# Performance work log

Measured on AMD Instinct MI355X. Metric: run time of the kernel, lower is better.

The kernel has to match this reference:

```python
import jax, jax.numpy as jnp
import numpy as np

B, T, C, H = 4, 2048, 1024, 16
D = C // H  # head dim = 64


def _layernorm(x, g, b, eps=1e-5):
    mu = jnp.mean(x, axis=-1, keepdims=True)
    var = jnp.var(x, axis=-1, keepdims=True)
    return (x - mu) * jax.lax.rsqrt(var + eps) * g + b


def setup_inputs() -> dict:
    key = jax.random.key(0)
    ks = jax.random.split(key, 8)
    s = 0.02
    return {
        "x": jax.random.normal(ks[0], (B, T, C), dtype=jnp.float32),
        "ln1_g": jnp.ones((C,), jnp.float32),
        "ln1_b": jnp.zeros((C,), jnp.float32),
        "W_qkv": jax.random.normal(ks[1], (C, 3 * C), dtype=jnp.float32) * s,
        "b_qkv": jnp.zeros((3 * C,), jnp.float32),
        "W_o": jax.random.normal(ks[2], (C, C), dtype=jnp.float32) * s,
        "b_o": jnp.zeros((C,), jnp.float32),
        "ln2_g": jnp.ones((C,), jnp.float32),
        "ln2_b": jnp.zeros((C,), jnp.float32),
        "W_fc": jax.random.normal(ks[3], (C, 4 * C), dtype=jnp.float32) * s,
        "b_fc": jnp.zeros((4 * C,), jnp.float32),
        "W_pr": jax.random.normal(ks[4], (4 * C, C), dtype=jnp.float32) * s,
        "b_pr": jnp.zeros((C,), jnp.float32),
    }


def reference(x, ln1_g, ln1_b, W_qkv, b_qkv, W_o, b_o, ln2_g, ln2_b, W_fc, b_fc, W_pr, b_pr):
    # --- attention sub-block ---
    h = _layernorm(x, ln1_g, ln1_b)
    qkv = h @ W_qkv + b_qkv                       # [B,T,3C]
    q, k, v = jnp.split(qkv, 3, axis=-1)
    q = q.reshape(B, T, H, D).transpose(0, 2, 1, 3)  # [B,H,T,D]
    k = k.reshape(B, T, H, D).transpose(0, 2, 1, 3)
    v = v.reshape(B, T, H, D).transpose(0, 2, 1, 3)
    att = jnp.einsum("bhqd,bhkd->bhqk", q, k) * (1.0 / jnp.sqrt(jnp.float32(D)))
    causal = jnp.tril(jnp.ones((T, T), dtype=bool))
    att = jnp.where(causal, att, jnp.float32(-jnp.inf))
    att = jax.nn.softmax(att, axis=-1)
    y = jnp.einsum("bhqk,bhkd->bhqd", att, v)     # [B,H,T,D]
    y = y.transpose(0, 2, 1, 3).reshape(B, T, C)
    y = y @ W_o + b_o
    x = x + y
    # --- FFN sub-block ---
    h2 = _layernorm(x, ln2_g, ln2_b)
    f = jax.nn.gelu(h2 @ W_fc + b_fc, approximate=False)  # nn.GELU default = exact
    f = f @ W_pr + b_pr
    return x + f
```

## Files before the change

### kernel.cpp

```cpp
#include <hip/hip_runtime.h>
#include <math.h>

#define Bz 4
#define Tz 2048
#define Cz 1024
#define Hz 16
#define Dz 64
#define MTOK (Bz*Tz)

typedef __attribute__((ext_vector_type(8))) short short8;
typedef __attribute__((ext_vector_type(4))) short short4v;
typedef __attribute__((ext_vector_type(4))) float f32x4;

typedef unsigned int u32_g __attribute__((address_space(1)));
typedef unsigned int u32_l __attribute__((address_space(3)));

__device__ __forceinline__ unsigned short f2bf(float f) {
    unsigned int u = __float_as_uint(f);
    u += 0x7fffu + ((u >> 16) & 1u);
    return (unsigned short)(u >> 16);
}
__device__ __forceinline__ float bf2f(unsigned short h) {
    return __uint_as_float((unsigned int)h << 16);
}

__device__ __forceinline__ void async_cp16(const unsigned short* g, unsigned short* l) {
    __builtin_amdgcn_global_load_lds((const u32_g*)g, (u32_l*)l, 16, 0, 0);
}

#define BARX() __builtin_amdgcn_s_barrier()
#define LGKM0() do { asm volatile("s_waitcnt lgkmcnt(0)" ::: "memory"); __builtin_amdgcn_sched_barrier(0); } while (0)
#define VMC(n) asm volatile("s_waitcnt vmcnt(" #n ")" ::: "memory")

__global__ void transpose_w(const float* __restrict__ W, unsigned short* __restrict__ Wt,
                            int K, int N) {
    __shared__ float tile[32][33];
    int n0 = blockIdx.x * 32, k0 = blockIdx.y * 32;
    int tx = threadIdx.x, ty = threadIdx.y;
    #pragma unroll
    for (int i = 0; i < 4; i++)
        tile[ty + i * 8][tx] = W[(size_t)(k0 + ty + i * 8) * N + n0 + tx];
    __syncthreads();
    #pragma unroll
    for (int i = 0; i < 4; i++)
        Wt[(size_t)(n0 + ty + i * 8) * K + k0 + tx] = f2bf(tile[tx][ty + i * 8]);
}

__global__ void ln_kernel(const float* __restrict__ x, const float* __restrict__ g,
                          const float* __restrict__ bb, unsigned short* __restrict__ out) {
    int tok = blockIdx.x, tid = threadIdx.x;
    const float4 v = ((const float4*)(x + (size_t)tok * Cz))[tid];
    float s = v.x + v.y + v.z + v.w;
    float sq = v.x * v.x + v.y * v.y + v.z * v.z + v.w * v.w;
    #pragma unroll
    for (int m = 1; m < 64; m <<= 1) { s += __shfl_xor(s, m); sq += __shfl_xor(sq, m); }
    __shared__ float red[8];
    int lane = tid & 63, wid = tid >> 6;
    if (!lane) { red[wid] = s; red[4 + wid] = sq; }
    __syncthreads();
    s = red[0] + red[1] + red[2] + red[3];
    sq = red[4] + red[5] + red[6] + red[7];
    float mu = s * (1.0f / Cz);
    float var = sq * (1.0f / Cz) - mu * mu;
    float rs = rsqrtf(var + 1e-5f);
    float4 gv = ((const float4*)g)[tid];
    float4 bv = ((const float4*)bb)[tid];
    short4v o;
    o[0] = f2bf((v.x - mu) * rs * gv.x + bv.x);
    o[1] = f2bf((v.y - mu) * rs * gv.y + bv.y);
    o[2] = f2bf((v.z - mu) * rs * gv.z + bv.z);
    o[3] = f2bf((v.w - mu) * rs * gv.w + bv.w);
    *(short4v*)(out + (size_t)tok * Cz + tid * 4) = o;
}

#define MODE_QKV 0
#define MODE_RESID 1
#define MODE_GELU 2

template <int MODE>
__device__ __forceinline__ void write_elem(int row, int col, float val, int N,
                                           float* __restrict__ outf, unsigned short* __restrict__ outb,
                                           const float* __restrict__ resid,
                                           unsigned short* __restrict__ qo, unsigned short* __restrict__ ko,
                                           unsigned short* __restrict__ vo) {
    if constexpr (MODE == MODE_QKV) {
        int which = col >> 10, cc = col & 1023;
        int hh = cc >> 6, dd = cc & 63;
        int b_ = row >> 11, t = row & 2047;
        if (which == 2) {
            vo[((size_t)(b_ * Hz + hh) * Dz + dd) * Tz + t] = f2bf(val);
        } else {
            unsigned short* dst = which ? ko : qo;
            dst[((size_t)(b_ * Hz + hh) * Tz + t) * Dz + dd] = f2bf(val);
        }
    } else if constexpr (MODE == MODE_RESID) {
        size_t idx = (size_t)row * N + col;
        outf[idx] = val + resid[idx];
    } else {
        float c = val * (1.0f + 0.044715f * val * val);
        float e = __expf(1.5957691216057308f * c);
        outb[(size_t)row * N + col] = f2bf(val * e / (1.0f + e));
    }
}

template <int MODE>
__launch_bounds__(512, 1)
__global__ void gemm8_n256(const unsigned short* __restrict__ A, const unsigned short* __restrict__ Bt,
                           int lda, int K, int N, const float* __restrict__ bias,
                           float* __restrict__ outf, unsigned short* __restrict__ outb,
                           const float* __restrict__ resid,
                           unsigned short* __restrict__ qo, unsigned short* __restrict__ ko,
                           unsigned short* __restrict__ vo) {
    __shared__ __align__(16) unsigned short As[2][2][256 * 32];
    __shared__ __align__(16) unsigned short Bs[2][2][256 * 32];
    const int tid = threadIdx.x;
    const int lane = tid & 63;
    const int wid = tid >> 6;
    const int quad = lane >> 4, l15 = lane & 15;
    const int gm = wid >> 2, gn = wid & 3;
    const int id = blockIdx.x;
    const int rr = id >> 3;
    const int m0 = ((id & 7) * 4 + (rr & 3)) * 256;
    const int n0 = (rr >> 2) * 256;
    const int NT = K >> 6;

    const int srow = tid >> 2;
    const int lseg = (tid & 3) ^ ((tid >> 3) & 3);
    const unsigned short* Ag0 = A + (size_t)(m0 + srow) * lda + lseg * 8;
    const unsigned short* Ag1 = A + (size_t)(m0 + 128 + srow) * lda + lseg * 8;
    const unsigned short* Bg0 = Bt + (size_t)(n0 + srow) * lda + lseg * 8;
    const unsigned short* Bg1 = Bt + (size_t)(n0 + 128 + srow) * lda + lseg * 8;

    f32x4 acc[8][4] = {};
    short8 af[8], bf[4];

#define STA(bufd, kkd, tt) do { \
    async_cp16(Ag0 + (size_t)(tt) * 64 + (kkd) * 32, &As[bufd][kkd][tid * 8]); \
    async_cp16(Ag1 + (size_t)(tt) * 64 + (kkd) * 32, &As[bufd][kkd][4096 + tid * 8]); } while (0)
#define STB(bufd, kkd, tt) do { \
    async_cp16(Bg0 + (size_t)(tt) * 64 + (kkd) * 32, &Bs[bufd][kkd][tid * 8]); \
    async_cp16(Bg1 + (size_t)(tt) * 64 + (kkd) * 32, &Bs[bufd][kkd][4096 + tid * 8]); } while (0)
#define RDA(kkd) do { _Pragma("unroll") for (int mi = 0; mi < 8; mi++) { \
    const int ra = gm * 128 + mi * 16 + l15; \
    af[mi] = *(const short8*)&As[buf][kkd][ra * 32 + ((quad ^ ((ra >> 1) & 3)) << 3)]; } } while (0)
#define RDB2(kkd, nia, nib) do { \
    { const int rb = gn * 64 + (nia) * 16 + l15; \
      bf[nia] = *(const short8*)&Bs[buf][kkd][rb * 32 + ((quad ^ ((rb >> 1) & 3)) << 3)]; } \
    { const int rb = gn * 64 + (nib) * 16 + l15; \
      bf[nib] = *(const short8*)&Bs[buf][kkd][rb * 32 + ((quad ^ ((rb >> 1) & 3)) << 3)]; } } while (0)
#define MM2(nia, nib) do { _Pragma("unroll") for (int mi = 0; mi < 8; mi++) { \
    acc[mi][nia] = __builtin_amdgcn_mfma_f32_16x16x32_bf16(af[mi], bf[nia], acc[mi][nia], 0, 0, 0); \
    acc[mi][nib] = __builtin_amdgcn_mfma_f32_16x16x32_bf16(af[mi], bf[nib], acc[mi][nib], 0, 0, 0); } } while (0)

    STA(0, 0, 0); STB(0, 0, 0);
    STA(0, 1, 0); STB(0, 1, 0);
    STA(1, 0, 1); STB(1, 0, 1);
    VMC(8);
    BARX();

    for (int t = 0; t < NT; t++) {
        const int buf = t & 1;
        const int nb = buf ^ 1;
        RDA(0); RDB2(0, 0, 1);
        if (t + 1 < NT) STA(nb, 1, t + 1);
        BARX(); LGKM0();
        __builtin_amdgcn_s_setprio(1);
        MM2(0, 1);
        __builtin_amdgcn_s_setprio(0);
        BARX();
        RDB2(0, 2, 3);
        if (t + 1 < NT) STB(nb, 1, t + 1);
        BARX(); LGKM0();
        __builtin_amdgcn_s_setprio(1);
        MM2(2, 3);
        __builtin_amdgcn_s_setprio(0);
        if (t + 1 < NT) { VMC(8); } else { VMC(0); }
        BARX();
        RDA(1); RDB2(1, 0, 1);
        if (t + 2 < NT) STA(buf, 0, t + 2);
        BARX(); LGKM0();
        __builtin_amdgcn_s_setprio(1);
        MM2(0, 1);
        __builtin_amdgcn_s_setprio(0);
        BARX();
        RDB2(1, 2, 3);
        if (t + 2 < NT) STB(buf, 0, t + 2);
        BARX(); LGKM0();
        __builtin_amdgcn_s_setprio(1);
        MM2(2, 3);
        __builtin_amdgcn_s_setprio(0);
        if (t + 2 < NT) { VMC(8); } else if (t + 1 < NT) { VMC(4); } else { VMC(0); }
        BARX();
    }
#undef STA
#undef STB
#undef RDA
#undef RDB2
#undef MM2

    #pragma unroll
    for (int ni = 0; ni < 4; ni++) {
        const int col = n0 + gn * 64 + ni * 16 + l15;
        const float bv = bias[col];
        #pragma unroll
        for (int mi = 0; mi < 8; mi++) {
            #pragma unroll
            for (int r = 0; r < 4; r++) {
                const int row = m0 + gm * 128 + mi * 16 + quad * 4 + r;
                write_elem<MODE>(row, col, acc[mi][ni][r] + bv, N, outf, outb, resid, qo, ko, vo);
            }
        }
    }
}

template <int MODE>
__launch_bounds__(512, 1)
__global__ void gemm8_n128(const unsigned short* __restrict__ A, const unsigned short* __restrict__ Bt,
                           int lda, int K, int N, const float* __restrict__ bias,
                           float* __restrict__ outf, unsigned short* __restrict__ outb,
                           const float* __restrict__ resid,
                           unsigned short* __restrict__ qo, unsigned short* __restrict__ ko,
                           unsigned short* __restrict__ vo) {
    __shared__ __align__(16) unsigned short As[2][2][256 * 32];
    __shared__ __align__(16) unsigned short Bs[2][2][128 * 32];
    const int tid = threadIdx.x;
    const int lane = tid & 63;
    const int wid = tid >> 6;
    const int quad = lane >> 4, l15 = lane & 15;
    const int gm = wid >> 1, gn = wid & 1;
    const int id = blockIdx.x;
    const int rr = id >> 3;
    const int m0 = ((id & 7) * 4 + (rr & 3)) * 256;
    const int n0 = (rr >> 2) * 128;
    const int NT = K >> 6;

    const int srow = tid >> 2;
    const int lseg = (tid & 3) ^ ((tid >> 3) & 3);
    const unsigned short* Ag0 = A + (size_t)(m0 + srow) * lda + lseg * 8;
    const unsigned short* Ag1 = A + (size_t)(m0 + 128 + srow) * lda + lseg * 8;
    const unsigned short* Bg0 = Bt + (size_t)(n0 + srow) * lda + lseg * 8;

    f32x4 acc[4][4] = {};
    short8 af[4], bf[4];

#define STA(bufd, kkd, tt) do { \
    async_cp16(Ag0 + (size_t)(tt) * 64 + (kkd) * 32, &As[bufd][kkd][tid * 8]); \
    async_cp16(Ag1 + (size_t)(tt) * 64 + (kkd) * 32, &As[bufd][kkd][4096 + tid * 8]); } while (0)
#define STB(bufd, kkd, tt) \
    async_cp16(Bg0 + (size_t)(tt) * 64 + (kkd) * 32, &Bs[bufd][kkd][tid * 8])
#define RDA(kkd) do { _Pragma("unroll") for (int mi = 0; mi < 4; mi++) { \
    const int ra = gm * 64 + mi * 16 + l15; \
    af[mi] = *(const short8*)&As[buf][kkd][ra * 32 + ((quad ^ ((ra >> 1) & 3)) << 3)]; } } while (0)
#define RDB(kkd) do { _Pragma("unroll") for (int ni = 0; ni < 4; ni++) { \
    const int rb = gn * 64 + ni * 16 + l15; \
    bf[ni] = *(const short8*)&Bs[buf][kkd][rb * 32 + ((quad ^ ((rb >> 1) & 3)) << 3)]; } } while (0)
#define MM16() do { _Pragma("unroll") for (int mi = 0; mi < 4; mi++) \
    _Pragma("unroll") for (int ni = 0; ni < 4; ni++) \
        acc[mi][ni] = __builtin_amdgcn_mfma_f32_16x16x32_bf16(af[mi], bf[ni], acc[mi][ni], 0, 0, 0); } while (0)

    STA(0, 0, 0); STB(0, 0, 0);
    STA(0, 1, 0); STB(0, 1, 0);
    STA(1, 0, 1); STB(1, 0, 1);
    VMC(6);
    BARX();

    for (int t = 0; t < NT; t++) {
        const int buf = t & 1;
        const int nb = buf ^ 1;
        RDA(0); RDB(0);
        if (t + 1 < NT) { STA(nb, 1, t + 1); STB(nb, 1, t + 1); }
        BARX(); LGKM0();
        __builtin_amdgcn_s_setprio(1);
        MM16();
        __builtin_amdgcn_s_setprio(0);
        if (t + 1 < NT) { VMC(6); } else { VMC(0); }
        BARX();
        RDA(1); RDB(1);
        if (t + 2 < NT) { STA(buf, 0, t + 2); STB(buf, 0, t + 2); }
        BARX(); LGKM0();
        __builtin_amdgcn_s_setprio(1);
        MM16();
        __builtin_amdgcn_s_setprio(0);
        if (t + 2 < NT) { VMC(6); } else if (t + 1 < NT) { VMC(3); } else { VMC(0); }
        BARX();
    }
#undef STA
#undef STB
#undef RDA
#undef RDB
#undef MM16

    #pragma unroll
    for (int ni = 0; ni < 4; ni++) {
        const int col = n0 + gn * 64 + ni * 16 + l15;
        const float bv = bias[col];
        #pragma unroll
        for (int mi = 0; mi < 4; mi++) {
            #pragma unroll
            for (int r = 0; r < 4; r++) {
                const int row = m0 + gm * 64 + mi * 16 + quad * 4 + r;
                write_elem<MODE>(row, col, acc[mi][ni][r] + bv, N, outf, outb, resid, qo, ko, vo);
            }
        }
    }
}

#define ATT_SC 0.18033688011112042f
__launch_bounds__(256)
__global__ void attn_kernel(const unsigned short* __restrict__ qb, const unsigned short* __restrict__ kb,
                            const unsigned short* __restrict__ vt, unsigned short* __restrict__ y) {
    __shared__ __align__(16) unsigned short Klds[64 * 64];
    __shared__ __align__(16) unsigned short Vtl[64 * 64];
    __shared__ __align__(16) unsigned short Plds[4][16 * 72];
    const int tid = threadIdx.x;
    const int lane = tid & 63, wid = tid >> 6;
    const int quad = lane >> 4, l15 = lane & 15;
    const int bh = blockIdx.x & 63;
    const int qt = 15 - (int)(blockIdx.x >> 6);
    const size_t baseT = (size_t)bh * Tz;
    const size_t vbase = (size_t)bh * Dz;
    const int qb0 = qt * 128;

    short8 qf[2][2];
    {
        const unsigned short* q0p = qb + (baseT + qb0 + wid * 16 + l15) * Dz + quad * 8;
        qf[0][0] = *(const short8*)q0p;
        qf[0][1] = *(const short8*)(q0p + 32);
        const unsigned short* q1p = q0p + (size_t)64 * Dz;
        qf[1][0] = *(const short8*)q1p;
        qf[1][1] = *(const short8*)(q1p + 32);
    }

    f32x4 o[2][4] = {};
    float lsum[2][4] = {{0.f,0.f,0.f,0.f},{0.f,0.f,0.f,0.f}};

    const int srow = lane >> 3;
    const int swz = ((lane & 7) ^ srow) * 8;
    const unsigned short* kg0 = kb + (baseT + wid * 8 + srow) * Dz + swz;
    const unsigned short* kg1 = kg0 + (size_t)32 * Dz;
    const unsigned short* vg0 = vt + (vbase + wid * 8 + srow) * Tz + swz;
    const unsigned short* vg1 = vg0 + (size_t)32 * Tz;
    unsigned short* kl0 = &Klds[wid * 512 + lane * 8];
    unsigned short* kl1 = kl0 + 2048;
    unsigned short* vl0 = &Vtl[wid * 512 + lane * 8];
    unsigned short* vl1 = vl0 + 2048;

    const int nchunk = 2 * qt + 2;

    for (int ci = 0; ci < nchunk; ci++) {
        const int k0 = ci * 64;
        async_cp16(kg0 + (size_t)k0 * Dz, kl0);
        async_cp16(kg1 + (size_t)k0 * Dz, kl1);
        async_cp16(vg0 + k0, vl0);
        async_cp16(vg1 + k0, vl1);
        __syncthreads();

        #pragma unroll
        for (int t = 0; t < 2; t++) {
            if (t == 0 && ci == nchunk - 1) continue;
            const bool diag = (ci == nchunk - 2 + t);

            f32x4 s[4];
            #pragma unroll
            for (int c = 0; c < 4; c++) {
                const int rk = c * 16 + l15;
                short8 kf0 = *(const short8*)&Klds[rk * 64 + ((quad ^ (rk & 7)) * 8)];
                short8 kf1 = *(const short8*)&Klds[rk * 64 + (((quad + 4) ^ (rk & 7)) * 8)];
                f32x4 z = {};
                z = __builtin_amdgcn_mfma_f32_16x16x32_bf16(qf[t][0], kf0, z, 0, 0, 0);
                s[c] = __builtin_amdgcn_mfma_f32_16x16x32_bf16(qf[t][1], kf1, z, 0, 0, 0);
            }
            const int qr = qb0 + t * 64 + wid * 16 + quad * 4;
            #pragma unroll
            for (int c = 0; c < 4; c++)
                #pragma unroll
                for (int r = 0; r < 4; r++) {
                    float p = exp2f(s[c][r] * ATT_SC);
                    if (diag) {
                        int key = k0 + c * 16 + l15;
                        p = (key <= qr + r) ? p : 0.f;
                    }
                    s[c][r] = p;
                    lsum[t][r] += p;
                }
            unsigned short* P = Plds[wid];
            #pragma unroll
            for (int c = 0; c < 4; c++)
                #pragma unroll
                for (int r = 0; r < 4; r++)
                    P[(quad * 4 + r) * 72 + c * 16 + l15] = f2bf(s[c][r]);
            short8 pf0 = *(const short8*)&P[l15 * 72 + quad * 8];
            short8 pf1 = *(const short8*)&P[l15 * 72 + 32 + quad * 8];
            #pragma unroll
            for (int nc = 0; nc < 4; nc++) {
                const int rv = nc * 16 + l15;
                short8 vf0 = *(const short8*)&Vtl[rv * 64 + ((quad ^ (rv & 7)) * 8)];
                short8 vf1 = *(const short8*)&Vtl[rv * 64 + (((quad + 4) ^ (rv & 7)) * 8)];
                o[t][nc] = __builtin_amdgcn_mfma_f32_16x16x32_bf16(pf0, vf0, o[t][nc], 0, 0, 0);
                o[t][nc] = __builtin_amdgcn_mfma_f32_16x16x32_bf16(pf1, vf1, o[t][nc], 0, 0, 0);
            }
        }
        __syncthreads();
    }

    const int b_ = bh >> 4, hh = bh & 15;
    #pragma unroll
    for (int t = 0; t < 2; t++)
        #pragma unroll
        for (int r = 0; r < 4; r++) {
            float ls = lsum[t][r];
            #pragma unroll
            for (int m = 1; m < 16; m <<= 1) ls += __shfl_xor(ls, m);
            float inv = 1.0f / ls;
            size_t tok = (size_t)qb0 + t * 64 + wid * 16 + quad * 4 + r;
            unsigned short* yr = y + ((size_t)b_ * Tz + tok) * Cz + hh * Dz;
            #pragma unroll
            for (int nc = 0; nc < 4; nc++)
                yr[nc * 16 + l15] = f2bf(o[t][nc][r] * inv);
        }
}

extern "C" void kernel_launch(void* const* d_in, const int* in_sizes, int n_in,
                              void* d_out, int out_size, void* d_ws, size_t ws_size,
                              hipStream_t stream) {
    const float* x    = (const float*)d_in[0];
    const float* ln1g = (const float*)d_in[1];
    const float* ln1b = (const float*)d_in[2];
    const float* Wqkv = (const float*)d_in[3];
    const float* bqkv = (const float*)d_in[4];
    const float* Wo   = (const float*)d_in[5];
    const float* bo   = (const float*)d_in[6];
    const float* ln2g = (const float*)d_in[7];
    const float* ln2b = (const float*)d_in[8];
    const float* Wfc  = (const float*)d_in[9];
    const float* bfc  = (const float*)d_in[10];
    const float* Wpr  = (const float*)d_in[11];
    const float* bpr  = (const float*)d_in[12];
    float* out = (float*)d_out;

    char* ws = (char*)d_ws;
    size_t off = 0;
    auto alloc = [&](size_t bytes) { void* p = ws + off; off += (bytes + 255) & ~(size_t)255; return p; };
    unsigned short* wqkv_t = (unsigned short*)alloc((size_t)3072 * 1024 * 2);
    unsigned short* wo_t   = (unsigned short*)alloc((size_t)1024 * 1024 * 2);
    unsigned short* wfc_t  = (unsigned short*)alloc((size_t)4096 * 1024 * 2);
    unsigned short* wpr_t  = (unsigned short*)alloc((size_t)1024 * 4096 * 2);
    unsigned short* h1     = (unsigned short*)alloc((size_t)MTOK * Cz * 2);
    unsigned short* qbuf   = (unsigned short*)alloc((size_t)MTOK * Cz * 2);
    unsigned short* kbuf   = (unsigned short*)alloc((size_t)MTOK * Cz * 2);
    unsigned short* vbuf   = (unsigned short*)alloc((size_t)MTOK * Cz * 2);
    unsigned short* ybuf   = (unsigned short*)alloc((size_t)MTOK * Cz * 2);
    float*          x1     = (float*)alloc((size_t)MTOK * Cz * 4);
    unsigned short* h2     = (unsigned short*)alloc((size_t)MTOK * Cz * 2);
    unsigned short* fbuf   = (unsigned short*)alloc((size_t)MTOK * 4096 * 2);

    dim3 tb(32, 8);
    transpose_w<<<dim3(3072 / 32, 1024 / 32), tb, 0, stream>>>(Wqkv, wqkv_t, 1024, 3072);
    transpose_w<<<dim3(1024 / 32, 1024 / 32), tb, 0, stream>>>(Wo, wo_t, 1024, 1024);
    transpose_w<<<dim3(4096 / 32, 1024 / 32), tb, 0, stream>>>(Wfc, wfc_t, 1024, 4096);
    transpose_w<<<dim3(1024 / 32, 4096 / 32), tb, 0, stream>>>(Wpr, wpr_t, 4096, 1024);

    ln_kernel<<<MTOK, 256, 0, stream>>>(x, ln1g, ln1b, h1);
    gemm8_n256<MODE_QKV><<<384, 512, 0, stream>>>(h1, wqkv_t, 1024, 1024, 3072, bqkv,
                                                  nullptr, nullptr, nullptr, qbuf, kbuf, vbuf);
    attn_kernel<<<1024, 256, 0, stream>>>(qbuf, kbuf, vbuf, ybuf);
    gemm8_n128<MODE_RESID><<<256, 512, 0, stream>>>(ybuf, wo_t, 1024, 1024, 1024, bo,
                                                    x1, nullptr, x, nullptr, nullptr, nullptr);
    ln_kernel<<<MTOK, 256, 0, stream>>>(x1, ln2g, ln2b, h2);
    gemm8_n256<MODE_GELU><<<512, 512, 0, stream>>>(h2, wfc_t, 1024, 1024, 4096, bfc,
                                                   nullptr, fbuf, nullptr, nullptr, nullptr, nullptr);
    gemm8_n128<MODE_RESID><<<256, 512, 0, stream>>>(fbuf, wpr_t, 4096, 4096, 1024, bpr,
                                                    out, nullptr, x1, nullptr, nullptr, nullptr);
}
```

Measured before the change: 564.7 us.

## Restructure GEMM pipeline with one-stage prefetch and transpose V separately

The GEMM main loops now prefetch only the next K-tile into the alternate buffer, without the previous two-ahead scheme. The last iteration is peeled out of the loop. Explicit lgkmcnt waits are replaced by sched_barrier fences, and the n256 kernel loads A fragments in two halves of four to cut register pressure. The QKV epilogue now writes V in the same row-major layout as Q and K, into scratch reusing fbuf, and a separate transpose kernel produces the D-major V layout. The aim is to avoid strided scattered stores in the epilogue, at the cost of one extra kernel launch and an extra pass over V.

```diff
diff --git a/kernel.cpp b/kernel.cpp
--- a/kernel.cpp
+++ b/kernel.cpp
@@ -29,8 +29,8 @@
 }
 
 #define BARX() __builtin_amdgcn_s_barrier()
-#define LGKM0() do { asm volatile("s_waitcnt lgkmcnt(0)" ::: "memory"); __builtin_amdgcn_sched_barrier(0); } while (0)
-#define VMC(n) asm volatile("s_waitcnt vmcnt(" #n ")" ::: "memory")
+#define VMC(n) asm volatile("s_waitcnt vmcnt(" #n ")" ::: )
+#define SCHEDF() __builtin_amdgcn_sched_barrier(0x7F)
 
 __global__ void transpose_w(const float* __restrict__ W, unsigned short* __restrict__ Wt,
                             int K, int N) {
@@ -44,6 +44,30 @@
     #pragma unroll
     for (int i = 0; i < 4; i++)
         Wt[(size_t)(n0 + ty + i * 8) * K + k0 + tx] = f2bf(tile[tx][ty + i * 8]);
+}
+
+__global__ void transpose_v(const unsigned short* __restrict__ in, unsigned short* __restrict__ out) {
+    __shared__ unsigned short tile[64][68];
+    const int bh = blockIdx.x;
+    const int t0 = blockIdx.y * 64;
+    const int tid = threadIdx.x;
+    const int r4 = tid >> 4;
+    const int c4 = tid & 15;
+    #pragma unroll
+    for (int p = 0; p < 4; p++) {
+        const int r = p * 16 + r4;
+        *(short4v*)&tile[r][c4 * 4] =
+            *(const short4v*)&in[((size_t)bh * Tz + t0 + r) * Dz + c4 * 4];
+    }
+    __syncthreads();
+    #pragma unroll
+    for (int p = 0; p < 4; p++) {
+        const int d = p * 16 + r4;
+        short4v o;
+        #pragma unroll
+        for (int j = 0; j < 4; j++) o[j] = tile[c4 * 4 + j][d];
+        *(short4v*)&out[((size_t)bh * Dz + d) * Tz + t0 + c4 * 4] = o;
+    }
 }
 
 __global__ void ln_kernel(const float* __restrict__ x, const float* __restrict__ g,
@@ -87,12 +111,8 @@
         int which = col >> 10, cc = col & 1023;
         int hh = cc >> 6, dd = cc & 63;
         int b_ = row >> 11, t = row & 2047;
-        if (which == 2) {
-            vo[((size_t)(b_ * Hz + hh) * Dz + dd) * Tz + t] = f2bf(val);
-        } else {
-            unsigned short* dst = which ? ko : qo;
-            dst[((size_t)(b_ * Hz + hh) * Tz + t) * Dz + dd] = f2bf(val);
-        }
+        unsigned short* dst = (which == 0) ? qo : (which == 1) ? ko : vo;
+        dst[((size_t)(b_ * Hz + hh) * Tz + t) * Dz + dd] = f2bf(val);
     } else if constexpr (MODE == MODE_RESID) {
         size_t idx = (size_t)row * N + col;
         outf[idx] = val + resid[idx];
@@ -124,15 +144,15 @@
     const int n0 = (rr >> 2) * 256;
     const int NT = K >> 6;
 
+    const int lseg = (tid & 3) ^ ((tid >> 3) & 3);
     const int srow = tid >> 2;
-    const int lseg = (tid & 3) ^ ((tid >> 3) & 3);
     const unsigned short* Ag0 = A + (size_t)(m0 + srow) * lda + lseg * 8;
     const unsigned short* Ag1 = A + (size_t)(m0 + 128 + srow) * lda + lseg * 8;
     const unsigned short* Bg0 = Bt + (size_t)(n0 + srow) * lda + lseg * 8;
     const unsigned short* Bg1 = Bt + (size_t)(n0 + 128 + srow) * lda + lseg * 8;
 
     f32x4 acc[8][4] = {};
-    short8 af[8], bf[4];
+    short8 af[4], bf[4];
 
 #define STA(bufd, kkd, tt) do { \
     async_cp16(Ag0 + (size_t)(tt) * 64 + (kkd) * 32, &As[bufd][kkd][tid * 8]); \
@@ -140,63 +160,83 @@
 #define STB(bufd, kkd, tt) do { \
     async_cp16(Bg0 + (size_t)(tt) * 64 + (kkd) * 32, &Bs[bufd][kkd][tid * 8]); \
     async_cp16(Bg1 + (size_t)(tt) * 64 + (kkd) * 32, &Bs[bufd][kkd][4096 + tid * 8]); } while (0)
-#define RDA(kkd) do { _Pragma("unroll") for (int mi = 0; mi < 8; mi++) { \
-    const int ra = gm * 128 + mi * 16 + l15; \
-    af[mi] = *(const short8*)&As[buf][kkd][ra * 32 + ((quad ^ ((ra >> 1) & 3)) << 3)]; } } while (0)
-#define RDB2(kkd, nia, nib) do { \
-    { const int rb = gn * 64 + (nia) * 16 + l15; \
-      bf[nia] = *(const short8*)&Bs[buf][kkd][rb * 32 + ((quad ^ ((rb >> 1) & 3)) << 3)]; } \
-    { const int rb = gn * 64 + (nib) * 16 + l15; \
-      bf[nib] = *(const short8*)&Bs[buf][kkd][rb * 32 + ((quad ^ ((rb >> 1) & 3)) << 3)]; } } while (0)
-#define MM2(nia, nib) do { _Pragma("unroll") for (int mi = 0; mi < 8; mi++) { \
-    acc[mi][nia] = __builtin_amdgcn_mfma_f32_16x16x32_bf16(af[mi], bf[nia], acc[mi][nia], 0, 0, 0); \
-    acc[mi][nib] = __builtin_amdgcn_mfma_f32_16x16x32_bf16(af[mi], bf[nib], acc[mi][nib], 0, 0, 0); } } while (0)
+#define RDA4(kkd, mb) do { _Pragma("unroll") for (int j = 0; j < 4; j++) { \
+    const int ra = gm * 128 + ((mb) + j) * 16 + l15; \
+    af[j] = *(const short8*)&As[buf][kkd][ra * 32 + ((quad ^ ((ra >> 1) & 3)) << 3)]; } } while (0)
+#define RDB4(kkd) do { _Pragma("unroll") for (int j = 0; j < 4; j++) { \
+    const int rb = gn * 64 + j * 16 + l15; \
+    bf[j] = *(const short8*)&Bs[buf][kkd][rb * 32 + ((quad ^ ((rb >> 1) & 3)) << 3)]; } } while (0)
+#define MFMA16(mb) do { _Pragma("unroll") for (int j = 0; j < 4; j++) \
+    _Pragma("unroll") for (int ni = 0; ni < 4; ni++) \
+        acc[(mb) + j][ni] = __builtin_amdgcn_mfma_f32_16x16x32_bf16(af[j], bf[ni], acc[(mb) + j][ni], 0, 0, 0); } while (0)
 
     STA(0, 0, 0); STB(0, 0, 0);
     STA(0, 1, 0); STB(0, 1, 0);
-    STA(1, 0, 1); STB(1, 0, 1);
-    VMC(8);
+    VMC(4);
+    SCHEDF();
     BARX();
 
-    for (int t = 0; t < NT; t++) {
+    for (int t = 0; t < NT - 1; t++) {
         const int buf = t & 1;
         const int nb = buf ^ 1;
-        RDA(0); RDB2(0, 0, 1);
-        if (t + 1 < NT) STA(nb, 1, t + 1);
-        BARX(); LGKM0();
+        RDA4(0, 0); RDB4(0);
+        STA(nb, 0, t + 1);
+        BARX();
         __builtin_amdgcn_s_setprio(1);
-        MM2(0, 1);
+        MFMA16(0);
         __builtin_amdgcn_s_setprio(0);
         BARX();
-        RDB2(0, 2, 3);
-        if (t + 1 < NT) STB(nb, 1, t + 1);
-        BARX(); LGKM0();
+        RDA4(0, 4);
+        STB(nb, 0, t + 1);
+        BARX();
         __builtin_amdgcn_s_setprio(1);
-        MM2(2, 3);
+        MFMA16(4);
         __builtin_amdgcn_s_setprio(0);
-        if (t + 1 < NT) { VMC(8); } else { VMC(0); }
-        BARX();
-        RDA(1); RDB2(1, 0, 1);
-        if (t + 2 < NT) STA(buf, 0, t + 2);
-        BARX(); LGKM0();
+        VMC(4);
+        SCHEDF();
+        BARX();
+        RDA4(1, 0); RDB4(1);
+        STA(nb, 1, t + 1);
+        BARX();
         __builtin_amdgcn_s_setprio(1);
-        MM2(0, 1);
+        MFMA16(0);
         __builtin_amdgcn_s_setprio(0);
         BARX();
-        RDB2(1, 2, 3);
-        if (t + 2 < NT) STB(buf, 0, t + 2);
-        BARX(); LGKM0();
+        RDA4(1, 4);
+        STB(nb, 1, t + 1);
+        BARX();
         __builtin_amdgcn_s_setprio(1);
-        MM2(2, 3);
+        MFMA16(4);
         __builtin_amdgcn_s_setprio(0);
-        if (t + 2 < NT) { VMC(8); } else if (t + 1 < NT) { VMC(4); } else { VMC(0); }
-        BARX();
+        VMC(4);
+        SCHEDF();
+        BARX();
+    }
+    {
+        const int buf = (NT - 1) & 1;
+        RDA4(0, 0); RDB4(0);
+        BARX();
+        __builtin_amdgcn_s_setprio(1); MFMA16(0); __builtin_amdgcn_s_setprio(0);
+        BARX();
+        RDA4(0, 4);
+        BARX();
+        __builtin_amdgcn_s_setprio(1); MFMA16(4); __builtin_amdgcn_s_setprio(0);
+        VMC(0);
+        SCHEDF();
+        BARX();
+        RDA4(1, 0); RDB4(1);
+        BARX();
+        __builtin_amdgcn_s_setprio(1); MFMA16(0); __builtin_amdgcn_s_setprio(0);
+        BARX();
+        RDA4(1, 4);
+        BARX();
+        __builtin_amdgcn_s_setprio(1); MFMA16(4); __builtin_amdgcn_s_setprio(0);
     }
 #undef STA
 #undef STB
-#undef RDA
-#undef RDB2
-#undef MM2
+#undef RDA4
+#undef RDB4
+#undef MFMA16
 
     #pragma unroll
     for (int ni = 0; ni < 4; ni++) {
@@ -234,8 +274,8 @@
     const int n0 = (rr >> 2) * 128;
     const int NT = K >> 6;
 
+    const int lseg = (tid & 3) ^ ((tid >> 3) & 3);
     const int srow = tid >> 2;
-    const int lseg = (tid & 3) ^ ((tid >> 3) & 3);
     const unsigned short* Ag0 = A + (size_t)(m0 + srow) * lda + lseg * 8;
     const unsigned short* Ag1 = A + (size_t)(m0 + 128 + srow) * lda + lseg * 8;
     const unsigned short* Bg0 = Bt + (size_t)(n0 + srow) * lda + lseg * 8;
@@ -260,29 +300,43 @@
 
     STA(0, 0, 0); STB(0, 0, 0);
     STA(0, 1, 0); STB(0, 1, 0);
-    STA(1, 0, 1); STB(1, 0, 1);
-    VMC(6);
+    VMC(3);
+    SCHEDF();
     BARX();
 
-    for (int t = 0; t < NT; t++) {
+    for (int t = 0; t < NT - 1; t++) {
         const int buf = t & 1;
         const int nb = buf ^ 1;
         RDA(0); RDB(0);
-        if (t + 1 < NT) { STA(nb, 1, t + 1); STB(nb, 1, t + 1); }
-        BARX(); LGKM0();
+        STA(nb, 0, t + 1); STB(nb, 0, t + 1);
+        BARX();
         __builtin_amdgcn_s_setprio(1);
         MM16();
         __builtin_amdgcn_s_setprio(0);
-        if (t + 1 < NT) { VMC(6); } else { VMC(0); }
+        VMC(3);
+        SCHEDF();
         BARX();
         RDA(1); RDB(1);
-        if (t + 2 < NT) { STA(buf, 0, t + 2); STB(buf, 0, t + 2); }
-        BARX(); LGKM0();
+        STA(nb, 1, t + 1); STB(nb, 1, t + 1);
+        BARX();
         __builtin_amdgcn_s_setprio(1);
         MM16();
         __builtin_amdgcn_s_setprio(0);
-        if (t + 2 < NT) { VMC(6); } else if (t + 1 < NT) { VMC(3); } else { VMC(0); }
-        BARX();
+        VMC(3);
+        SCHEDF();
+        BARX();
+    }
+    {
+        const int buf = (NT - 1) & 1;
+        RDA(0); RDB(0);
+        BARX();
+        __builtin_amdgcn_s_setprio(1); MM16(); __builtin_amdgcn_s_setprio(0);
+        VMC(0);
+        SCHEDF();
+        BARX();
+        RDA(1); RDB(1);
+        BARX();
+        __builtin_amdgcn_s_setprio(1); MM16(); __builtin_amdgcn_s_setprio(0);
     }
 #undef STA
 #undef STB
@@ -453,6 +507,7 @@
     float*          x1     = (float*)alloc((size_t)MTOK * Cz * 4);
     unsigned short* h2     = (unsigned short*)alloc((size_t)MTOK * Cz * 2);
     unsigned short* fbuf   = (unsigned short*)alloc((size_t)MTOK * 4096 * 2);
+    unsigned short* vtmp   = fbuf;
 
     dim3 tb(32, 8);
     transpose_w<<<dim3(3072 / 32, 1024 / 32), tb, 0, stream>>>(Wqkv, wqkv_t, 1024, 3072);
@@ -462,7 +517,8 @@
 
     ln_kernel<<<MTOK, 256, 0, stream>>>(x, ln1g, ln1b, h1);
     gemm8_n256<MODE_QKV><<<384, 512, 0, stream>>>(h1, wqkv_t, 1024, 1024, 3072, bqkv,
-                                                  nullptr, nullptr, nullptr, qbuf, kbuf, vbuf);
+                                                  nullptr, nullptr, nullptr, qbuf, kbuf, vtmp);
+    transpose_v<<<dim3(64, 32), 256, 0, stream>>>(vtmp, vbuf);
     attn_kernel<<<1024, 256, 0, stream>>>(qbuf, kbuf, vbuf, ybuf);
     gemm8_n128<MODE_RESID><<<256, 512, 0, stream>>>(ybuf, wo_t, 1024, 1024, 1024, bo,
                                                     x1, nullptr, x, nullptr, nullptr, nullptr);
```

After: 555.6 us. Within noise of the previous version (-1.6%).
